# Optimization experiments

Hardware: AMD Instinct MI355X
Metric: run time of the kernel (lower is better)

The kernel has to match this reference:

```python
import jax, jax.numpy as jnp
import numpy as np
from math import sqrt

V, D, H, HD, L, F, P, NL = 32000, 768, 12, 64, 12, 3072, 2048, 2
B, S = 8, 1024
EPS = 1e-5


def setup_inputs() -> dict:
    key = jax.random.key(0)
    ks = jax.random.split(key, 12)
    n = lambda k, sh: (jax.random.normal(k, sh, jnp.float32) * 0.02)
    return {
        'tokens': jax.random.randint(ks[0], (B, S), 0, V, dtype=jnp.int32),
        'tok_emb': n(ks[1], (V, D)),
        'pos_emb': n(ks[2], (P, D)),
        'emb_ln_s': jnp.ones((D,), jnp.float32), 'emb_ln_b': jnp.zeros((D,), jnp.float32),
        'Wq': n(ks[3], (L, H, D, HD)), 'bq': jnp.zeros((L, H, HD), jnp.float32),
        'Wk': n(ks[4], (L, H, D, HD)), 'bk': jnp.zeros((L, H, HD), jnp.float32),
        'Wv': n(ks[5], (L, H, D, HD)), 'bv': jnp.zeros((L, H, HD), jnp.float32),
        'Wo': n(ks[6], (L, D, D)), 'bo': jnp.zeros((L, D), jnp.float32),
        'ln1_s': jnp.ones((L, D), jnp.float32), 'ln1_b': jnp.zeros((L, D), jnp.float32),
        'ln2_s': jnp.ones((L, D), jnp.float32), 'ln2_b': jnp.zeros((L, D), jnp.float32),
        'W1': n(ks[7], (L, D, F)), 'b1': jnp.zeros((L, F), jnp.float32),
        'W2': n(ks[8], (L, F, D)), 'b2': jnp.zeros((L, D), jnp.float32),
        'Wc': n(ks[9], (D, NL)), 'bc': jnp.zeros((NL,), jnp.float32),
    }


def _ln(x, s, b):
    m = jnp.mean(x, -1, keepdims=True)
    v = jnp.mean((x - m) ** 2, -1, keepdims=True)
    return (x - m) * jax.lax.rsqrt(v + EPS) * s + b


def reference(tokens, tok_emb, pos_emb, emb_ln_s, emb_ln_b,
              Wq, bq, Wk, bk, Wv, bv, Wo, bo,
              ln1_s, ln1_b, ln2_s, ln2_b, W1, b1, W2, b2, Wc, bc):
    b, s = tokens.shape
    # embeddings (dropout is eval-mode identity)
    x = tok_emb[tokens] + pos_emb[:s][None, :, :]          # [b, s, D]
    x = _ln(x, emb_ln_s, emb_ln_b)
    scale = 1.0 / sqrt(HD)
    for l in range(L):
        xn = _ln(x, ln1_s[l], ln1_b[l])
        q = jnp.einsum('bsd,hdk->bhsk', xn, Wq[l]) + bq[l][:, None, :]
        k = jnp.einsum('bsd,hdk->bhsk', xn, Wk[l]) + bk[l][:, None, :]
        v = jnp.einsum('bsd,hdk->bhsk', xn, Wv[l]) + bv[l][:, None, :]
        scores = jnp.einsum('bhsk,bhtk->bhst', q, k) * scale   # [b,H,s,s]
        w = jax.nn.softmax(scores, axis=-1)
        o = jnp.einsum('bhst,bhtk->bhsk', w, v)                # [b,H,s,HD]
        o = o.transpose(0, 2, 1, 3).reshape(b, s, D)           # concat heads
        x = x + o @ Wo[l] + bo[l]
        xn = _ln(x, ln2_s[l], ln2_b[l])
        h = jax.nn.gelu(xn @ W1[l] + b1[l], approximate=False)
        x = x + h @ W2[l] + b2[l]
    # CLS token -> classifier (dropout identity)
    return x[:, 0, :] @ Wc + bc                                # [b, NL]
```

## Files before the change

kernel.cpp:

```cpp
#include <hip/hip_runtime.h>
#include <hip/hip_bf16.h>
#include <math.h>

#define B_   8
#define S_   1024
#define D_   768
#define H_   12
#define HD_  64
#define L_   12
#define F_   3072
#define NTOK 8192

typedef __bf16 bf16x8 __attribute__((ext_vector_type(8)));
typedef float  f32x4  __attribute__((ext_vector_type(4)));
typedef unsigned short u16;

static __device__ __forceinline__ unsigned short f2bf_bits(float f) {
    __hip_bfloat16 h = __float2bfloat16(f);
    return __builtin_bit_cast(unsigned short, h);
}
static __device__ __forceinline__ float bf2f(unsigned short u) {
    unsigned int t = ((unsigned int)u) << 16;
    return __builtin_bit_cast(float, t);
}
static __device__ __forceinline__ void gload16(const void* g, void* l) {
    __builtin_amdgcn_global_load_lds(
        (__attribute__((address_space(1))) void*)g,
        (__attribute__((address_space(3))) void*)l, 16, 0, 0);
}

__global__ __launch_bounds__(256)
void prep_ln_kernel(const float* __restrict__ Wq, const float* __restrict__ Wk,
                    const float* __restrict__ Wv, const float* __restrict__ Wo,
                    const float* __restrict__ W1, const float* __restrict__ W2,
                    int l, __hip_bfloat16* __restrict__ wbuf,
                    const float* __restrict__ xin, const float* __restrict__ gam,
                    const float* __restrict__ bet, __hip_bfloat16* __restrict__ xnout)
{
    __shared__ u16 T[64][68];
    if (blockIdx.x >= 1728) {
        const int row  = (blockIdx.x - 1728)*4 + (threadIdx.x >> 6);
        const int lane = threadIdx.x & 63;
        const float* xr = xin + (size_t)row * D_;
        float v[12]; float s1 = 0.f, s2 = 0.f;
#pragma unroll
        for (int c = 0; c < 3; ++c) {
            float4 t = *(const float4*)(xr + c*256 + lane*4);
            v[c*4+0]=t.x; v[c*4+1]=t.y; v[c*4+2]=t.z; v[c*4+3]=t.w;
            s1 += t.x+t.y+t.z+t.w;
            s2 += t.x*t.x + t.y*t.y + t.z*t.z + t.w*t.w;
        }
#pragma unroll
        for (int off = 32; off > 0; off >>= 1) { s1 += __shfl_xor(s1, off); s2 += __shfl_xor(s2, off); }
        const float mean = s1 * (1.f/768.f);
        const float rstd = rsqrtf(s2*(1.f/768.f) - mean*mean + 1e-5f);
        unsigned short* op = (unsigned short*)xnout + (size_t)row * D_;
#pragma unroll
        for (int c = 0; c < 3; ++c) {
            const int base = c*256 + lane*4;
            float4 g = *(const float4*)(gam + base);
            float4 bb = *(const float4*)(bet + base);
            ushort4 pk;
            pk.x = f2bf_bits((v[c*4+0]-mean)*rstd*g.x + bb.x);
            pk.y = f2bf_bits((v[c*4+1]-mean)*rstd*g.y + bb.y);
            pk.z = f2bf_bits((v[c*4+2]-mean)*rstd*g.z + bb.z);
            pk.w = f2bf_bits((v[c*4+3]-mean)*rstd*g.w + bb.w);
            *(ushort4*)(op + base) = pk;
        }
        return;
    }
    const int id = blockIdx.x;
    const float* src; __hip_bfloat16* dst;
    int R, C, r0, c0;
    if (id < 432) {
        int dtile = id % 12, t = id / 12;
        int which = t / 12, h = t % 12;
        src = (which == 0 ? Wq : which == 1 ? Wk : Wv) + (size_t)(l*12 + h) * 768 * 64;
        dst = wbuf + (size_t)(which*768 + h*64) * 768;
        R = 768; C = 64; r0 = dtile * 64; c0 = 0;
    } else if (id < 576) {
        int t = id - 432;
        src = Wo + (size_t)l * 768 * 768;
        dst = wbuf + 1769472;
        R = 768; C = 768; r0 = (t / 12) * 64; c0 = (t % 12) * 64;
    } else if (id < 1152) {
        int t = id - 576;
        src = W1 + (size_t)l * 768 * 3072;
        dst = wbuf + 2359296;
        R = 768; C = 3072; r0 = (t % 12) * 64; c0 = (t / 12) * 64;
    } else {
        int t = id - 1152;
        src = W2 + (size_t)l * 3072 * 768;
        dst = wbuf + 4718592;
        R = 3072; C = 768; r0 = (t / 12) * 64; c0 = (t % 12) * 64;
    }
    const int t = threadIdx.x;
    const int row = t >> 2, part = t & 3;
#pragma unroll
    for (int j = 0; j < 4; ++j) {
        const int c4 = (part + j*4) * 4;
        float4 v = *(const float4*)(src + (size_t)(r0 + row) * C + c0 + c4);
        T[c4+0][row] = f2bf_bits(v.x);
        T[c4+1][row] = f2bf_bits(v.y);
        T[c4+2][row] = f2bf_bits(v.z);
        T[c4+3][row] = f2bf_bits(v.w);
    }
    __syncthreads();
    const int c = t >> 2;
    u16* drow = (u16*)dst + (size_t)(c0 + c) * R + r0;
#pragma unroll
    for (int j = 0; j < 4; ++j) {
        const int r4 = (part + j*4) * 4;
        ushort4 pk = *(const ushort4*)&T[c][r4];
        *(ushort4*)(drow + r4) = pk;
    }
}

__global__ __launch_bounds__(256)
void prep_bqkv_kernel(const float* __restrict__ bq, const float* __restrict__ bk,
                      const float* __restrict__ bv, float* __restrict__ bqkv)
{
    int i = blockIdx.x * 256 + threadIdx.x;
    int l = i / 2304, c = i % 2304;
    int which = c / 768, hk = c % 768;
    const float* src = which == 0 ? bq : which == 1 ? bk : bv;
    bqkv[i] = src[l*768 + hk];
}

__global__ __launch_bounds__(256)
void embed_ln_kernel(const int* __restrict__ tokens, const float* __restrict__ tok_emb,
                     const float* __restrict__ pos_emb, const float* __restrict__ gam,
                     const float* __restrict__ bet, float* __restrict__ x)
{
    const int row  = blockIdx.x*4 + (threadIdx.x >> 6);
    const int lane = threadIdx.x & 63;
    const int s    = row & (S_-1);
    const int tok  = tokens[row];
    const float* te = tok_emb + (size_t)tok * D_;
    const float* pe = pos_emb + (size_t)s   * D_;
    float v[12]; float s1 = 0.f, s2 = 0.f;
#pragma unroll
    for (int c = 0; c < 3; ++c) {
        const int base = c*256 + lane*4;
        float4 a = *(const float4*)(te + base);
        float4 p = *(const float4*)(pe + base);
        float t0 = a.x+p.x, t1 = a.y+p.y, t2 = a.z+p.z, t3 = a.w+p.w;
        v[c*4+0]=t0; v[c*4+1]=t1; v[c*4+2]=t2; v[c*4+3]=t3;
        s1 += t0+t1+t2+t3;
        s2 += t0*t0 + t1*t1 + t2*t2 + t3*t3;
    }
#pragma unroll
    for (int off = 32; off > 0; off >>= 1) { s1 += __shfl_xor(s1, off); s2 += __shfl_xor(s2, off); }
    const float mean = s1 * (1.f/768.f);
    const float rstd = rsqrtf(s2*(1.f/768.f) - mean*mean + 1e-5f);
    float* xr = x + (size_t)row * D_;
#pragma unroll
    for (int c = 0; c < 3; ++c) {
        const int base = c*256 + lane*4;
        float4 g = *(const float4*)(gam + base);
        float4 bb = *(const float4*)(bet + base);
        float4 o;
        o.x = (v[c*4+0]-mean)*rstd*g.x + bb.x;
        o.y = (v[c*4+1]-mean)*rstd*g.y + bb.y;
        o.z = (v[c*4+2]-mean)*rstd*g.z + bb.z;
        o.w = (v[c*4+3]-mean)*rstd*g.w + bb.w;
        *(float4*)(xr + base) = o;
    }
}

__global__ __launch_bounds__(256)
void ln_kernel(const float* __restrict__ xin, const float* __restrict__ gam,
               const float* __restrict__ bet, __hip_bfloat16* __restrict__ out)
{
    const int row  = blockIdx.x*4 + (threadIdx.x >> 6);
    const int lane = threadIdx.x & 63;
    const float* xr = xin + (size_t)row * D_;
    float v[12]; float s1 = 0.f, s2 = 0.f;
#pragma unroll
    for (int c = 0; c < 3; ++c) {
        float4 t = *(const float4*)(xr + c*256 + lane*4);
        v[c*4+0]=t.x; v[c*4+1]=t.y; v[c*4+2]=t.z; v[c*4+3]=t.w;
        s1 += t.x+t.y+t.z+t.w;
        s2 += t.x*t.x + t.y*t.y + t.z*t.z + t.w*t.w;
    }
#pragma unroll
    for (int off = 32; off > 0; off >>= 1) { s1 += __shfl_xor(s1, off); s2 += __shfl_xor(s2, off); }
    const float mean = s1 * (1.f/768.f);
    const float rstd = rsqrtf(s2*(1.f/768.f) - mean*mean + 1e-5f);
    unsigned short* op = (unsigned short*)out + (size_t)row * D_;
#pragma unroll
    for (int c = 0; c < 3; ++c) {
        const int base = c*256 + lane*4;
        float4 g = *(const float4*)(gam + base);
        float4 bb = *(const float4*)(bet + base);
        ushort4 pk;
        pk.x = f2bf_bits((v[c*4+0]-mean)*rstd*g.x + bb.x);
        pk.y = f2bf_bits((v[c*4+1]-mean)*rstd*g.y + bb.y);
        pk.z = f2bf_bits((v[c*4+2]-mean)*rstd*g.z + bb.z);
        pk.w = f2bf_bits((v[c*4+3]-mean)*rstd*g.w + bb.w);
        *(ushort4*)(op + base) = pk;
    }
}

template<int EPI>
__global__ __launch_bounds__(512, 2)
void gemm256_kernel(const __hip_bfloat16* __restrict__ A,
                    const __hip_bfloat16* __restrict__ Bt,
                    const float* __restrict__ bias,
                    __hip_bfloat16* __restrict__ outb,
                    __hip_bfloat16* __restrict__ outv,
                    int N, int K, int nTiles)
{
    __shared__ __align__(16) char smem[49152];
    char* const As0 = smem;
    char* const As1 = smem + 16384;
    char* const Bs0 = smem + 32768;
    char* const Bs1 = smem + 40960;

    const int tid  = threadIdx.x;
    const int lane = tid & 63;
    const int wid  = tid >> 6;

    const int nwg   = gridDim.x;
    const int chunk = nwg >> 3;
    const int bid   = blockIdx.x;
    const int swz   = (bid & 7) * chunk + (bid >> 3);
    const int m0 = (swz / nTiles) * 256;
    const int n0 = (swz % nTiles) * 128;

    const int l4 = lane >> 2;
    const int sswz = ((lane & 3) ^ ((l4 >> 1) & 3)) * 8;
    const __hip_bfloat16* aSrc = A  + (size_t)(m0 + wid*16 + l4) * K + sswz;
    const __hip_bfloat16* bSrc = Bt + (size_t)(n0 + wid*16 + l4) * K + sswz;
    const int sOff = wid*1024 + lane*16;

    f32x4 acc[4][4] = {};
    const int wm = wid >> 1, wn = wid & 1;
    const int cl = lane & 15, hi = lane >> 4;

    int aoff[4], boff[4];
#pragma unroll
    for (int m = 0; m < 4; ++m) {
        const int row = wm*64 + m*16 + cl;
        aoff[m] = row*64 + ((hi ^ ((row >> 1) & 3)) << 4);
    }
#pragma unroll
    for (int n = 0; n < 4; ++n) {
        const int row = wn*64 + n*16 + cl;
        boff[n] = row*64 + ((hi ^ ((row >> 1) & 3)) << 4);
    }

    auto STAGE = [&](char* aBuf, char* bBuf, int kt) {
        gload16(aSrc + kt,                  aBuf + sOff);
        gload16(aSrc + kt + (size_t)128*K,  aBuf + 8192 + sOff);
        gload16(bSrc + kt,                  bBuf + sOff);
    };

    const int NT = K >> 5;
    STAGE(As0, Bs0, 0);
    STAGE(As1, Bs1, 32);

    for (int t = 0; t < NT; ++t) {
        if (t < NT - 1) asm volatile("s_waitcnt vmcnt(3)" ::: "memory");
        else            asm volatile("s_waitcnt vmcnt(0)" ::: "memory");
        __builtin_amdgcn_s_barrier();

        char* const ac = (t & 1) ? As1 : As0;
        char* const bc = (t & 1) ? Bs1 : Bs0;
        bf16x8 af[4], bfr[4];
#pragma unroll
        for (int m = 0; m < 4; ++m) af[m]  = *(const bf16x8*)(ac + aoff[m]);
#pragma unroll
        for (int n = 0; n < 4; ++n) bfr[n] = *(const bf16x8*)(bc + boff[n]);
        asm volatile("s_waitcnt lgkmcnt(0)" ::: "memory");
        __builtin_amdgcn_sched_barrier(0);
        __builtin_amdgcn_s_barrier();

        if (t + 2 < NT) STAGE(ac, bc, (t + 2) << 5);

        __builtin_amdgcn_s_setprio(1);
#pragma unroll
        for (int m = 0; m < 4; ++m)
#pragma unroll
            for (int n = 0; n < 4; ++n)
                acc[m][n] = __builtin_amdgcn_mfma_f32_16x16x32_bf16(af[m], bfr[n], acc[m][n], 0, 0, 0);
        __builtin_amdgcn_s_setprio(0);
    }

    const bool vpath = (EPI == 0) && (n0 >= 1536);

    if (!vpath) {
        const int strideN = (EPI == 0) ? 1536 : N;
#pragma unroll
        for (int half = 0; half < 2; ++half) {
            __syncthreads();
            if ((wm >> 1) == half) {
#pragma unroll
                for (int n = 0; n < 4; ++n) {
                    const int col2 = wn*64 + n*16 + cl;
                    const float bv = bias[n0 + col2];
#pragma unroll
                    for (int m = 0; m < 4; ++m) {
#pragma unroll
                        for (int i = 0; i < 4; ++i) {
                            const int row = (wm & 1)*64 + m*16 + hi*4 + i;
                            float v = acc[m][n][i] + bv;
                            if constexpr (EPI == 1) {
                                const float y = 0.7978845608f * (v + 0.044715f*v*v*v);
                                const float e = __expf(-2.0f * fabsf(y));
                                const float th = (1.0f - e) / (1.0f + e);
                                v = 0.5f * v * (1.0f + copysignf(th, y));
                            }
                            *(u16*)(smem + row*256 + ((((col2 >> 3) ^ (row & 15))) << 4)
                                         + ((col2 & 7) << 1)) = f2bf_bits(v);
                        }
                    }
                }
            }
            __syncthreads();
            const int r = tid >> 2;
            const int part = tid & 3;
            char* dst = (char*)outb + ((size_t)(m0 + half*128 + r) * strideN + n0) * 2;
#pragma unroll
            for (int j = 0; j < 4; ++j) {
                const int ch = part + j*4;
                float4 vv = *(const float4*)(smem + r*256 + ((ch ^ (r & 15)) << 4));
                *(float4*)(dst + ch*16) = vv;
            }
        }
    } else {
        const int hdbase = n0 - 1536;
        const int bb = m0 >> 10;
#pragma unroll
        for (int half = 0; half < 2; ++half) {
            __syncthreads();
            if ((wm >> 1) == half) {
#pragma unroll
                for (int n = 0; n < 4; ++n) {
                    const int hdl = wn*64 + n*16 + cl;
                    const float bv = bias[n0 + hdl];
#pragma unroll
                    for (int m = 0; m < 4; ++m) {
                        const int sl = (wm & 1)*64 + m*16 + hi*4;
                        ushort4 pk;
                        pk.x = f2bf_bits(acc[m][n][0] + bv);
                        pk.y = f2bf_bits(acc[m][n][1] + bv);
                        pk.z = f2bf_bits(acc[m][n][2] + bv);
                        pk.w = f2bf_bits(acc[m][n][3] + bv);
                        *(ushort4*)(smem + hdl*256 + ((((sl >> 3) ^ (hdl & 15))) << 4)
                                         + (sl & 7)*2) = pk;
                    }
                }
            }
            __syncthreads();
            const int hdl2 = tid >> 2;
            const int q4   = tid & 3;
            u16* dst = (u16*)outv + ((size_t)(bb*768) + hdbase + hdl2)*1024
                                  + (m0 & 1023) + half*128;
#pragma unroll
            for (int j = 0; j < 4; ++j) {
                const int ch = q4*4 + j;
                const int slot = ch ^ (hdl2 & 15);
                *(float4*)((char*)dst + ch*16) = *(const float4*)(smem + hdl2*256 + (slot << 4));
            }
        }
    }
}

__global__ __launch_bounds__(256)
void gemm_res_kernel(const __hip_bfloat16* __restrict__ A,
                     const __hip_bfloat16* __restrict__ Bt,
                     const float* __restrict__ bias,
                     float* __restrict__ outf,
                     int N, int K, int nTiles)
{
    __shared__ __align__(16) char smem[49152];
    char* const As0 = smem;
    char* const As1 = smem + 8192;
    char* const Bs0 = smem + 16384;
    char* const Bs1 = smem + 32768;

    const int tid  = threadIdx.x;
    const int lane = tid & 63;
    const int wid  = tid >> 6;

    const int nwg   = gridDim.x;
    const int chunk = nwg >> 3;
    const int bid   = blockIdx.x;
    const int swz   = (bid & 7) * chunk + (bid >> 3);
    const int m0 = (swz / nTiles) * 64;
    const int n0 = (swz % nTiles) * 128;

    const int lrow = lane >> 3;
    const int scol = ((lane & 7) ^ lrow) * 8;
    const __hip_bfloat16* aSrc = A  + (size_t)(m0 + wid*16 + lrow) * K + scol;
    const __hip_bfloat16* bSrc = Bt + (size_t)(n0 + wid*32 + lrow) * K + scol;
    const int aOff = wid*2048 + lane*16;
    const int bOff = wid*4096 + lane*16;

    f32x4 acc[2][4] = {};
    const int wm = wid >> 1, wn = wid & 1;
    const int cl = lane & 15, hi = lane >> 4;

    auto STAGE = [&](char* aBuf, char* bBuf, int kt) {
#pragma unroll
        for (int i = 0; i < 2; ++i)
            gload16(aSrc + kt + (size_t)i*8*K, aBuf + aOff + i*1024);
#pragma unroll
        for (int i = 0; i < 4; ++i)
            gload16(bSrc + kt + (size_t)i*8*K, bBuf + bOff + i*1024);
    };

    const int NT = K >> 6;
    STAGE(As0, Bs0, 0);
    STAGE(As1, Bs1, 64);

    for (int t = 0; t < NT; ++t) {
        if (t < NT - 1) asm volatile("s_waitcnt vmcnt(6)" ::: "memory");
        else            asm volatile("s_waitcnt vmcnt(0)" ::: "memory");
        __builtin_amdgcn_s_barrier();

        char* const ac = (t & 1) ? As1 : As0;
        char* const bc = (t & 1) ? Bs1 : Bs0;
        bf16x8 af[2][2], bfr[2][4];
#pragma unroll
        for (int kk = 0; kk < 2; ++kk) {
#pragma unroll
            for (int m = 0; m < 2; ++m) {
                const int row  = wm*32 + m*16 + cl;
                const int slot = ((kk<<2) + hi) ^ (row & 7);
                af[kk][m] = *(const bf16x8*)(ac + row*128 + slot*16);
            }
#pragma unroll
            for (int n = 0; n < 4; ++n) {
                const int row  = wn*64 + n*16 + cl;
                const int slot = ((kk<<2) + hi) ^ (row & 7);
                bfr[kk][n] = *(const bf16x8*)(bc + row*128 + slot*16);
            }
        }
        asm volatile("s_waitcnt lgkmcnt(0)" ::: "memory");
        __builtin_amdgcn_sched_barrier(0);
        __builtin_amdgcn_s_barrier();

        if (t + 2 < NT) STAGE(ac, bc, (t + 2) << 6);

        __builtin_amdgcn_s_setprio(1);
#pragma unroll
        for (int kk = 0; kk < 2; ++kk)
#pragma unroll
            for (int m = 0; m < 2; ++m)
#pragma unroll
                for (int n = 0; n < 4; ++n)
                    acc[m][n] = __builtin_amdgcn_mfma_f32_16x16x32_bf16(af[kk][m], bfr[kk][n], acc[m][n], 0, 0, 0);
        __builtin_amdgcn_s_setprio(0);
    }

    __syncthreads();

#pragma unroll
    for (int n = 0; n < 4; ++n) {
        const int col = wn*64 + n*16 + cl;
        const float bv = bias[n0 + col];
#pragma unroll
        for (int m = 0; m < 2; ++m) {
#pragma unroll
            for (int i = 0; i < 4; ++i) {
                const int row = wm*32 + m*16 + hi*4 + i;
                *(float*)(smem + row*512 + ((((col >> 2) ^ (row & 31))) << 4)
                               + ((col & 3) << 2)) = acc[m][n][i] + bv;
            }
        }
    }
    __syncthreads();
    const int r = tid >> 2;
    const int part = tid & 3;
    float* drow = outf + (size_t)(m0 + r) * N + n0;
#pragma unroll
    for (int j = 0; j < 8; ++j) {
        const int ch = part + j*4;
        f32x4 vv = *(const f32x4*)(smem + r*512 + ((ch ^ (r & 31)) << 4));
        float* dp = drow + ch*4;
        f32x4 g = *(const f32x4*)dp;
        g += vv;
        *(f32x4*)dp = g;
    }
}

__global__ __launch_bounds__(512)
void attn_kernel(const __hip_bfloat16* __restrict__ qkb, const __hip_bfloat16* __restrict__ vtb,
                 __hip_bfloat16* __restrict__ attno)
{
    __shared__ __align__(16) char Ks[2][8192];
    __shared__ __align__(16) char Vs[2][8192];
    __shared__ __align__(16) char Ps[16384];

    const u16* qk = (const u16*)qkb;
    const u16* vt = (const u16*)vtb;
    const int nwg = gridDim.x, bid = blockIdx.x, chunk = nwg >> 3;
    const int swz = (bid & 7) * chunk + (bid >> 3);
    const int bh = swz >> 3, qb = swz & 7;
    const int b = bh / H_, h = bh % H_;
    const int tid = threadIdx.x;
    const int lane = tid & 63, wid = tid >> 6;
    const int cl = lane & 15, hi = lane >> 4;
    const size_t browq = (size_t)(b*S_ + qb*128);

    bf16x8 qf[2];
    {
        const float qs = 0.1803368801f;
        const u16* qp = qk + (browq + wid*16 + cl)*1536 + h*64;
        u16 qt[16];
#pragma unroll
        for (int j = 0; j < 8; ++j) {
            qt[j]     = f2bf_bits(bf2f(qp[hi*8 + j]) * qs);
            qt[8 + j] = f2bf_bits(bf2f(qp[32 + hi*8 + j]) * qs);
        }
        qf[0] = *(const bf16x8*)&qt[0];
        qf[1] = *(const bf16x8*)&qt[8];
    }

    const int lrow = lane >> 3;
    const int scol = ((lane & 7) ^ lrow) * 8;
    const u16* kbase = qk + ((size_t)b*S_ + wid*8 + lrow)*1536 + 768 + h*64 + scol;
    const u16* vbase = vt + (((size_t)(b*H_ + h))*64 + wid*8 + lrow)*1024 + scol;
    const int ldst = wid*1024 + lane*16;

    char* pbase = Ps + wid*2048;
    char* paddr[4][4];
#pragma unroll
    for (int n = 0; n < 4; ++n)
#pragma unroll
        for (int i = 0; i < 4; ++i) {
            const int q = hi*4 + i;
            const int slot = (n*2 + (cl >> 3)) ^ (q & 7);
            paddr[n][i] = pbase + q*128 + slot*16 + (cl & 7)*2;
        }

    f32x4 acc_o[4] = {};
    float m_run = -1e30f;
    float l_part[4] = {0.f, 0.f, 0.f, 0.f};

    {
        gload16(kbase, Ks[0] + ldst);
        gload16(vbase, Vs[0] + ldst);
    }

    for (int t = 0; t < 16; ++t) {
        __syncthreads();
        if (t < 15) {
            const int nb = (t+1) & 1;
            gload16(kbase + (size_t)(t+1)*64*1536, Ks[nb] + ldst);
            gload16(vbase + (t+1)*64,              Vs[nb] + ldst);
        }
        const char* ks = Ks[t & 1];
        const char* vs = Vs[t & 1];

        f32x4 sc[4] = {};
#pragma unroll
        for (int kk = 0; kk < 2; ++kk) {
            bf16x8 kf[4];
#pragma unroll
            for (int n = 0; n < 4; ++n) {
                const int row = n*16 + cl;
                kf[n] = *(const bf16x8*)(ks + row*128 + (((kk*4 + hi) ^ (cl & 7)) << 4));
            }
#pragma unroll
            for (int n = 0; n < 4; ++n)
                sc[n] = __builtin_amdgcn_mfma_f32_16x16x32_bf16(qf[kk], kf[n], sc[n], 0, 0, 0);
        }

        float gmax;
        {
            float a0 = fmaxf(fmaxf(sc[0][0], sc[0][1]), fmaxf(sc[0][2], sc[0][3]));
            float a1 = fmaxf(fmaxf(sc[1][0], sc[1][1]), fmaxf(sc[1][2], sc[1][3]));
            float a2 = fmaxf(fmaxf(sc[2][0], sc[2][1]), fmaxf(sc[2][2], sc[2][3]));
            float a3 = fmaxf(fmaxf(sc[3][0], sc[3][1]), fmaxf(sc[3][2], sc[3][3]));
            gmax = fmaxf(fmaxf(a0, a1), fmaxf(a2, a3));
        }
        gmax = fmaxf(gmax, __shfl_xor(gmax, 1));
        gmax = fmaxf(gmax, __shfl_xor(gmax, 2));
        gmax = fmaxf(gmax, __shfl_xor(gmax, 4));
        gmax = fmaxf(gmax, __shfl_xor(gmax, 8));
        if (gmax > m_run + 5.7707801636f) {
            const float corr = exp2f(m_run - gmax);
            m_run = gmax;
#pragma unroll
            for (int i = 0; i < 4; ++i) l_part[i] *= corr;
#pragma unroll
            for (int nd = 0; nd < 4; ++nd)
#pragma unroll
                for (int i = 0; i < 4; ++i)
                    acc_o[nd][i] *= corr;
        }

#pragma unroll
        for (int n = 0; n < 4; ++n) {
#pragma unroll
            for (int i = 0; i < 4; ++i) {
                const float e = exp2f(sc[n][i] - m_run);
                l_part[i] += e;
                *(u16*)paddr[n][i] = f2bf_bits(e);
            }
        }

        asm volatile("s_waitcnt lgkmcnt(0)" ::: "memory");
        __builtin_amdgcn_sched_barrier(0);

#pragma unroll
        for (int kk = 0; kk < 2; ++kk) {
            const bf16x8 pf = *(const bf16x8*)(pbase + cl*128 + (((kk*4 + hi) ^ (cl & 7)) << 4));
            bf16x8 vf[4];
#pragma unroll
            for (int nd = 0; nd < 4; ++nd) {
                const int d = nd*16 + cl;
                vf[nd] = *(const bf16x8*)(vs + d*128 + (((kk*4 + hi) ^ (d & 7)) << 4));
            }
#pragma unroll
            for (int nd = 0; nd < 4; ++nd)
                acc_o[nd] = __builtin_amdgcn_mfma_f32_16x16x32_bf16(pf, vf[nd], acc_o[nd], 0, 0, 0);
        }
    }

    u16* op = (u16*)attno;
#pragma unroll
    for (int i = 0; i < 4; ++i) {
        float l = l_part[i];
        l += __shfl_xor(l, 1);
        l += __shfl_xor(l, 2);
        l += __shfl_xor(l, 4);
        l += __shfl_xor(l, 8);
        const float inv = 1.f / l;
        const size_t row = browq + wid*16 + hi*4 + i;
#pragma unroll
        for (int nd = 0; nd < 4; ++nd)
            op[row*768 + h*64 + nd*16 + cl] = f2bf_bits(acc_o[nd][i] * inv);
    }
}

__global__ __launch_bounds__(256)
void cls_kernel(const float* __restrict__ x, const float* __restrict__ Wc,
                const float* __restrict__ bc, float* __restrict__ out)
{
    const int b = blockIdx.x;
    const float* xr = x + (size_t)b * S_ * D_;
    float a0 = 0.f, a1 = 0.f;
    for (int d = threadIdx.x; d < 768; d += 256) {
        float xv = xr[d];
        a0 += xv * Wc[d*2+0];
        a1 += xv * Wc[d*2+1];
    }
#pragma unroll
    for (int off = 32; off > 0; off >>= 1) { a0 += __shfl_xor(a0, off); a1 += __shfl_xor(a1, off); }
    __shared__ float r0[4], r1[4];
    const int w = threadIdx.x >> 6;
    if ((threadIdx.x & 63) == 0) { r0[w] = a0; r1[w] = a1; }
    __syncthreads();
    if (threadIdx.x == 0) {
        out[b*2+0] = r0[0]+r0[1]+r0[2]+r0[3] + bc[0];
        out[b*2+1] = r1[0]+r1[1]+r1[2]+r1[3] + bc[1];
    }
}

extern "C" void kernel_launch(void* const* d_in, const int* in_sizes, int n_in,
                              void* d_out, int out_size, void* d_ws, size_t ws_size,
                              hipStream_t stream)
{
    const int*   tokens  = (const int*)  d_in[0];
    const float* tok_emb = (const float*)d_in[1];
    const float* pos_emb = (const float*)d_in[2];
    const float* e_s     = (const float*)d_in[3];
    const float* e_b     = (const float*)d_in[4];
    const float* Wq      = (const float*)d_in[5];
    const float* bq      = (const float*)d_in[6];
    const float* Wk      = (const float*)d_in[7];
    const float* bk      = (const float*)d_in[8];
    const float* Wv      = (const float*)d_in[9];
    const float* bv      = (const float*)d_in[10];
    const float* Wo      = (const float*)d_in[11];
    const float* bo      = (const float*)d_in[12];
    const float* l1s     = (const float*)d_in[13];
    const float* l1b     = (const float*)d_in[14];
    const float* l2s     = (const float*)d_in[15];
    const float* l2b     = (const float*)d_in[16];
    const float* W1      = (const float*)d_in[17];
    const float* b1      = (const float*)d_in[18];
    const float* W2      = (const float*)d_in[19];
    const float* b2      = (const float*)d_in[20];
    const float* Wc      = (const float*)d_in[21];
    const float* bc      = (const float*)d_in[22];
    (void)in_sizes; (void)n_in; (void)out_size;

    if (ws_size < 102346752) return;

    char* ws = (char*)d_ws;
    __hip_bfloat16* wbuf = (__hip_bfloat16*)(ws + 0);
    float*          bqkv = (float*)(ws + 14155776);
    float*          x    = (float*)(ws + 14266368);
    __hip_bfloat16* xn   = (__hip_bfloat16*)(ws + 39432192);
    __hip_bfloat16* qk   = (__hip_bfloat16*)(ws + 52015104);
    __hip_bfloat16* vT   = (__hip_bfloat16*)(ws + 77180928);
    __hip_bfloat16* att  = (__hip_bfloat16*)(ws + 89763840);
    __hip_bfloat16* hbuf = qk;

    __hip_bfloat16* wqkv_t = wbuf;
    __hip_bfloat16* wo_t   = wbuf + 1769472;
    __hip_bfloat16* w1_t   = wbuf + 2359296;
    __hip_bfloat16* w2_t   = wbuf + 4718592;

    prep_bqkv_kernel<<<108, 256, 0, stream>>>(bq, bk, bv, bqkv);
    embed_ln_kernel<<<2048, 256, 0, stream>>>(tokens, tok_emb, pos_emb, e_s, e_b, x);

    for (int l = 0; l < L_; ++l) {
        prep_ln_kernel<<<3776, 256, 0, stream>>>(Wq, Wk, Wv, Wo, W1, W2, l, wbuf,
                                                 x, l1s + l*768, l1b + l*768, xn);
        gemm256_kernel<0><<<576, 512, 0, stream>>>(xn, wqkv_t, bqkv + l*2304, qk, vT, 2304, 768, 18);
        attn_kernel<<<768, 512, 0, stream>>>(qk, vT, att);
        gemm_res_kernel<<<768, 256, 0, stream>>>(att, wo_t, bo + l*768, x, 768, 768, 6);
        ln_kernel<<<2048, 256, 0, stream>>>(x, l2s + l*768, l2b + l*768, xn);
        gemm256_kernel<1><<<768, 512, 0, stream>>>(xn, w1_t, b1 + l*3072, hbuf, nullptr, 3072, 768, 24);
        gemm_res_kernel<<<768, 256, 0, stream>>>(hbuf, w2_t, b2 + l*768, x, 768, 3072, 6);
    }
    cls_kernel<<<8, 256, 0, stream>>>(x, Wc, bc, (float*)d_out);
}
```

Measured before the change: 3.045 ms.

## Process two query tiles per wave in attention to reuse K/V fragments

Attention blocks now use 4 waves of 256 threads, each handling 32 query rows as two 16-row groups. K and V fragments read from LDS are reused across both groups, halving LDS fragment reads per MFMA and issuing more independent MFMAs per wave. Each thread also loads twice as many K/V rows. The exchange is higher register pressure (doubled accumulators and scores) and fewer waves per block for hiding latency.

```diff
diff --git a/kernel.cpp b/kernel.cpp
--- a/kernel.cpp
+++ b/kernel.cpp
@@ -486,7 +486,7 @@
     }
 }
 
-__global__ __launch_bounds__(512)
+__global__ __launch_bounds__(256)
 void attn_kernel(const __hip_bfloat16* __restrict__ qkb, const __hip_bfloat16* __restrict__ vtb,
                  __hip_bfloat16* __restrict__ attno)
 {
@@ -505,57 +505,55 @@
     const int cl = lane & 15, hi = lane >> 4;
     const size_t browq = (size_t)(b*S_ + qb*128);
 
-    bf16x8 qf[2];
-    {
+    bf16x8 qf[2][2];
+#pragma unroll
+    for (int g = 0; g < 2; ++g) {
         const float qs = 0.1803368801f;
-        const u16* qp = qk + (browq + wid*16 + cl)*1536 + h*64;
+        const u16* qp = qk + (browq + wid*32 + g*16 + cl)*1536 + h*64;
         u16 qt[16];
 #pragma unroll
         for (int j = 0; j < 8; ++j) {
             qt[j]     = f2bf_bits(bf2f(qp[hi*8 + j]) * qs);
             qt[8 + j] = f2bf_bits(bf2f(qp[32 + hi*8 + j]) * qs);
         }
-        qf[0] = *(const bf16x8*)&qt[0];
-        qf[1] = *(const bf16x8*)&qt[8];
+        qf[g][0] = *(const bf16x8*)&qt[0];
+        qf[g][1] = *(const bf16x8*)&qt[8];
     }
 
     const int lrow = lane >> 3;
     const int scol = ((lane & 7) ^ lrow) * 8;
-    const u16* kbase = qk + ((size_t)b*S_ + wid*8 + lrow)*1536 + 768 + h*64 + scol;
-    const u16* vbase = vt + (((size_t)(b*H_ + h))*64 + wid*8 + lrow)*1024 + scol;
-    const int ldst = wid*1024 + lane*16;
-
-    char* pbase = Ps + wid*2048;
-    char* paddr[4][4];
-#pragma unroll
-    for (int n = 0; n < 4; ++n)
-#pragma unroll
-        for (int i = 0; i < 4; ++i) {
-            const int q = hi*4 + i;
-            const int slot = (n*2 + (cl >> 3)) ^ (q & 7);
-            paddr[n][i] = pbase + q*128 + slot*16 + (cl & 7)*2;
-        }
-
-    f32x4 acc_o[4] = {};
+    const u16* kbase = qk + ((size_t)b*S_ + wid*16 + lrow)*1536 + 768 + h*64 + scol;
+    const u16* vbase = vt + (((size_t)(b*H_ + h))*64 + wid*16 + lrow)*1024 + scol;
+    const int ldst = wid*2048 + lane*16;
+
+    char* pbase = Ps + wid*4096;
+
+    f32x4 acc_o[2][4] = {};
     float m_run = -1e30f;
-    float l_part[4] = {0.f, 0.f, 0.f, 0.f};
+    float l_part[2][4] = {};
 
     {
-        gload16(kbase, Ks[0] + ldst);
-        gload16(vbase, Vs[0] + ldst);
+        gload16(kbase,                  Ks[0] + ldst);
+        gload16(kbase + (size_t)8*1536, Ks[0] + ldst + 1024);
+        gload16(vbase,                  Vs[0] + ldst);
+        gload16(vbase + 8*1024,         Vs[0] + ldst + 1024);
     }
 
     for (int t = 0; t < 16; ++t) {
         __syncthreads();
         if (t < 15) {
             const int nb = (t+1) & 1;
-            gload16(kbase + (size_t)(t+1)*64*1536, Ks[nb] + ldst);
-            gload16(vbase + (t+1)*64,              Vs[nb] + ldst);
+            const u16* kn = kbase + (size_t)(t+1)*64*1536;
+            const u16* vn = vbase + (t+1)*64;
+            gload16(kn,                  Ks[nb] + ldst);
+            gload16(kn + (size_t)8*1536, Ks[nb] + ldst + 1024);
+            gload16(vn,                  Vs[nb] + ldst);
+            gload16(vn + 8*1024,         Vs[nb] + ldst + 1024);
         }
         const char* ks = Ks[t & 1];
         const char* vs = Vs[t & 1];
 
-        f32x4 sc[4] = {};
+        f32x4 sc[2][4] = {};
 #pragma unroll
         for (int kk = 0; kk < 2; ++kk) {
             bf16x8 kf[4];
@@ -565,17 +563,23 @@
                 kf[n] = *(const bf16x8*)(ks + row*128 + (((kk*4 + hi) ^ (cl & 7)) << 4));
             }
 #pragma unroll
-            for (int n = 0; n < 4; ++n)
-                sc[n] = __builtin_amdgcn_mfma_f32_16x16x32_bf16(qf[kk], kf[n], sc[n], 0, 0, 0);
+            for (int g = 0; g < 2; ++g)
+#pragma unroll
+                for (int n = 0; n < 4; ++n)
+                    sc[g][n] = __builtin_amdgcn_mfma_f32_16x16x32_bf16(qf[g][kk], kf[n], sc[g][n], 0, 0, 0);
         }
 
         float gmax;
         {
-            float a0 = fmaxf(fmaxf(sc[0][0], sc[0][1]), fmaxf(sc[0][2], sc[0][3]));
-            float a1 = fmaxf(fmaxf(sc[1][0], sc[1][1]), fmaxf(sc[1][2], sc[1][3]));
-            float a2 = fmaxf(fmaxf(sc[2][0], sc[2][1]), fmaxf(sc[2][2], sc[2][3]));
-            float a3 = fmaxf(fmaxf(sc[3][0], sc[3][1]), fmaxf(sc[3][2], sc[3][3]));
-            gmax = fmaxf(fmaxf(a0, a1), fmaxf(a2, a3));
+            float a0 = fmaxf(fmaxf(sc[0][0][0], sc[0][0][1]), fmaxf(sc[0][0][2], sc[0][0][3]));
+#pragma unroll
+            for (int g = 0; g < 2; ++g)
+#pragma unroll
+                for (int n = 0; n < 4; ++n) {
+                    if (g == 0 && n == 0) continue;
+                    a0 = fmaxf(a0, fmaxf(fmaxf(sc[g][n][0], sc[g][n][1]), fmaxf(sc[g][n][2], sc[g][n][3])));
+                }
+            gmax = a0;
         }
         gmax = fmaxf(gmax, __shfl_xor(gmax, 1));
         gmax = fmaxf(gmax, __shfl_xor(gmax, 2));
@@ -585,21 +589,30 @@
             const float corr = exp2f(m_run - gmax);
             m_run = gmax;
 #pragma unroll
-            for (int i = 0; i < 4; ++i) l_part[i] *= corr;
-#pragma unroll
-            for (int nd = 0; nd < 4; ++nd)
-#pragma unroll
-                for (int i = 0; i < 4; ++i)
-                    acc_o[nd][i] *= corr;
-        }
-
-#pragma unroll
-        for (int n = 0; n < 4; ++n) {
-#pragma unroll
-            for (int i = 0; i < 4; ++i) {
-                const float e = exp2f(sc[n][i] - m_run);
-                l_part[i] += e;
-                *(u16*)paddr[n][i] = f2bf_bits(e);
+            for (int g = 0; g < 2; ++g)
+#pragma unroll
+                for (int i = 0; i < 4; ++i) l_part[g][i] *= corr;
+#pragma unroll
+            for (int g = 0; g < 2; ++g)
+#pragma unroll
+                for (int nd = 0; nd < 4; ++nd)
+#pragma unroll
+                    for (int i = 0; i < 4; ++i)
+                        acc_o[g][nd][i] *= corr;
+        }
+
+#pragma unroll
+        for (int g = 0; g < 2; ++g) {
+#pragma unroll
+            for (int n = 0; n < 4; ++n) {
+#pragma unroll
+                for (int i = 0; i < 4; ++i) {
+                    const float e = exp2f(sc[g][n][i] - m_run);
+                    l_part[g][i] += e;
+                    const int q = g*16 + hi*4 + i;
+                    const int slot = (n*2 + (cl >> 3)) ^ (q & 7);
+                    *(u16*)(pbase + q*128 + slot*16 + (cl & 7)*2) = f2bf_bits(e);
+                }
             }
         }
 
@@ -608,7 +621,12 @@
 
 #pragma unroll
         for (int kk = 0; kk < 2; ++kk) {
-            const bf16x8 pf = *(const bf16x8*)(pbase + cl*128 + (((kk*4 + hi) ^ (cl & 7)) << 4));
+            bf16x8 pf[2];
+#pragma unroll
+            for (int g = 0; g < 2; ++g) {
+                const int qrow = g*16 + cl;
+                pf[g] = *(const bf16x8*)(pbase + qrow*128 + (((kk*4 + hi) ^ (cl & 7)) << 4));
+            }
             bf16x8 vf[4];
 #pragma unroll
             for (int nd = 0; nd < 4; ++nd) {
@@ -616,24 +634,29 @@
                 vf[nd] = *(const bf16x8*)(vs + d*128 + (((kk*4 + hi) ^ (d & 7)) << 4));
             }
 #pragma unroll
+            for (int g = 0; g < 2; ++g)
+#pragma unroll
+                for (int nd = 0; nd < 4; ++nd)
+                    acc_o[g][nd] = __builtin_amdgcn_mfma_f32_16x16x32_bf16(pf[g], vf[nd], acc_o[g][nd], 0, 0, 0);
+        }
+    }
+
+    u16* op = (u16*)attno;
+#pragma unroll
+    for (int g = 0; g < 2; ++g) {
+#pragma unroll
+        for (int i = 0; i < 4; ++i) {
+            float l = l_part[g][i];
+            l += __shfl_xor(l, 1);
+            l += __shfl_xor(l, 2);
+            l += __shfl_xor(l, 4);
+            l += __shfl_xor(l, 8);
+            const float inv = 1.f / l;
+            const size_t row = browq + wid*32 + g*16 + hi*4 + i;
+#pragma unroll
             for (int nd = 0; nd < 4; ++nd)
-                acc_o[nd] = __builtin_amdgcn_mfma_f32_16x16x32_bf16(pf, vf[nd], acc_o[nd], 0, 0, 0);
-        }
-    }
-
-    u16* op = (u16*)attno;
-#pragma unroll
-    for (int i = 0; i < 4; ++i) {
-        float l = l_part[i];
-        l += __shfl_xor(l, 1);
-        l += __shfl_xor(l, 2);
-        l += __shfl_xor(l, 4);
-        l += __shfl_xor(l, 8);
-        const float inv = 1.f / l;
-        const size_t row = browq + wid*16 + hi*4 + i;
-#pragma unroll
-        for (int nd = 0; nd < 4; ++nd)
-            op[row*768 + h*64 + nd*16 + cl] = f2bf_bits(acc_o[nd][i] * inv);
+                op[row*768 + h*64 + nd*16 + cl] = f2bf_bits(acc_o[g][nd][i] * inv);
+        }
     }
 }
 
@@ -714,7 +737,7 @@
         prep_ln_kernel<<<3776, 256, 0, stream>>>(Wq, Wk, Wv, Wo, W1, W2, l, wbuf,
                                                  x, l1s + l*768, l1b + l*768, xn);
         gemm256_kernel<0><<<576, 512, 0, stream>>>(xn, wqkv_t, bqkv + l*2304, qk, vT, 2304, 768, 18);
-        attn_kernel<<<768, 512, 0, stream>>>(qk, vT, att);
+        attn_kernel<<<768, 256, 0, stream>>>(qk, vT, att);
         gemm_res_kernel<<<768, 256, 0, stream>>>(att, wo_t, bo + l*768, x, 768, 768, 6);
         ln_kernel<<<2048, 256, 0, stream>>>(x, l2s + l*768, l2b + l*768, xn);
         gemm256_kernel<1><<<768, 512, 0, stream>>>(xn, w1_t, b1 + l*3072, hbuf, nullptr, 3072, 768, 24);
```

After: 3.204 ms, median of 2. 1.05x slower.
